# Performance work log

Measured on AMD Instinct MI355X. Metric: run time of the kernel, lower is better.

The kernel has to match this reference:

```python
import jax, jax.numpy as jnp
import numpy as np

B, N, H, E, A, V, L = 64, 196, 512, 512, 512, 20000, 20


def setup_inputs() -> dict:
    key = jax.random.key(0)
    ks = jax.random.split(key, 16)
    s = lambda *sh: 0.02
    return {
        "encoder_outputs": jax.random.normal(ks[0], (B, N, H), dtype=jnp.float32),
        "captions": jax.random.randint(ks[1], (B, L), 0, V, dtype=jnp.int64),
        "emb": jax.random.normal(ks[2], (V, E), dtype=jnp.float32) * 0.02,
        "W_ih": jax.random.normal(ks[3], (4 * H, E + H), dtype=jnp.float32) * 0.02,
        "W_hh": jax.random.normal(ks[4], (4 * H, H), dtype=jnp.float32) * 0.02,
        "b_ih": jax.random.normal(ks[5], (4 * H,), dtype=jnp.float32) * 0.02,
        "b_hh": jax.random.normal(ks[6], (4 * H,), dtype=jnp.float32) * 0.02,
        "enc_W": jax.random.normal(ks[7], (A, H), dtype=jnp.float32) * 0.02,
        "enc_b": jax.random.normal(ks[8], (A,), dtype=jnp.float32) * 0.02,
        "dec_W": jax.random.normal(ks[9], (A, H), dtype=jnp.float32) * 0.02,
        "dec_b": jax.random.normal(ks[10], (A,), dtype=jnp.float32) * 0.02,
        "energy_W": jax.random.normal(ks[11], (1, A), dtype=jnp.float32) * 0.02,
        "energy_b": jax.random.normal(ks[12], (1,), dtype=jnp.float32) * 0.02,
        "fc_W": jax.random.normal(ks[13], (V, H), dtype=jnp.float32) * 0.02,
        "fc_b": jax.random.normal(ks[14], (V,), dtype=jnp.float32) * 0.02,
    }


def reference(encoder_outputs, captions, emb, W_ih, W_hh, b_ih, b_hh,
              enc_W, enc_b, dec_W, dec_b, energy_W, energy_b, fc_W, fc_b):
    b, max_len = captions.shape
    hid = W_hh.shape[1]
    vocab = fc_W.shape[0]
    dt = encoder_outputs.dtype

    # encoder projection is hidden-state independent: hoist out of the loop
    enc_proj = jnp.einsum('bnh,ah->bna', encoder_outputs, enc_W) + enc_b  # [B,N,A]
    # teacher forcing ratio = 1.0 => input at step t is captions[:, t-1]
    emb_seq = emb[captions[:, :-1]]                                      # [B,L-1,E]
    emb_seq = jnp.swapaxes(emb_seq, 0, 1)                                # [L-1,B,E]

    def step(carry, x_t):
        h, c = carry
        dec = h @ dec_W.T + dec_b                                        # [B,A]
        scores = jnp.tanh(enc_proj + dec[:, None, :]) @ energy_W[0] + energy_b[0]  # [B,N]
        attw = jax.nn.softmax(scores, axis=1)
        context = jnp.einsum('bn,bnh->bh', attw, encoder_outputs)        # [B,H]
        lstm_in = jnp.concatenate([x_t, context], axis=1)                # [B,E+H]
        gates = lstm_in @ W_ih.T + b_ih + h @ W_hh.T + b_hh              # [B,4H]
        i, f, g, o = jnp.split(gates, 4, axis=1)
        c_new = jax.nn.sigmoid(f) * c + jax.nn.sigmoid(i) * jnp.tanh(g)
        h_new = jax.nn.sigmoid(o) * jnp.tanh(c_new)
        out = h_new @ fc_W.T + fc_b                                      # [B,V]
        return (h_new, c_new), out

    h0 = jnp.zeros((b, hid), dtype=dt)
    c0 = jnp.zeros((b, hid), dtype=dt)
    (_, _), outs = jax.lax.scan(step, (h0, c0), emb_seq)                 # [L-1,B,V]
    outputs = jnp.concatenate(
        [jnp.zeros((b, 1, vocab), dtype=dt), jnp.swapaxes(outs, 0, 1)], axis=1)
    return outputs
```

## Files before the change

### kernel.cpp

```cpp
#include <hip/hip_runtime.h>
#include <hip/hip_bf16.h>
#include <math.h>

#define B   64
#define NN  196
#define HH  512
#define EE  512
#define AA  512
#define VV  20000
#define LL  20

typedef __attribute__((ext_vector_type(8))) short bf16x8;
typedef __attribute__((ext_vector_type(4))) float floatx4;

__device__ __forceinline__ float tanh_fast(float x) {
  float e2 = __expf(2.f * x);
  return 1.f - 2.f / (e2 + 1.f);
}
__device__ __forceinline__ float sigmoid_fast(float x) {
  return 1.f / (1.f + __expf(-x));
}
__device__ __forceinline__ float bf2f(unsigned short u) {
  return __uint_as_float(((unsigned)u) << 16);
}
__device__ __forceinline__ unsigned short f2bf(float v) {
  __hip_bfloat16 h = __float2bfloat16(v);
  return *reinterpret_cast<unsigned short*>(&h);
}

__device__ __forceinline__ unsigned ald(const unsigned* p) {
  return __hip_atomic_load(p, __ATOMIC_RELAXED, __HIP_MEMORY_SCOPE_AGENT);
}
__device__ __forceinline__ void ast(unsigned* p, unsigned v) {
  __hip_atomic_store(p, v, __ATOMIC_RELAXED, __HIP_MEMORY_SCOPE_AGENT);
}
__device__ __forceinline__ int aldi(const int* p) {
  return __hip_atomic_load(p, __ATOMIC_RELAXED, __HIP_MEMORY_SCOPE_AGENT);
}
__device__ __forceinline__ void asti(int* p, int v) {
  __hip_atomic_store(p, v, __ATOMIC_RELAXED, __HIP_MEMORY_SCOPE_AGENT);
}

__device__ __forceinline__ int ldsw(int row, int q4) {
  return (row * 4 + (q4 ^ ((row >> 1) & 3))) * 8;
}
__device__ __forceinline__ int ldsw8(int row, int q8) {
  return (row * 8 + (q8 ^ (row & 7))) * 8;
}

__global__ __launch_bounds__(256) void gemm_mfma_bt(
    const unsigned short* __restrict__ Xb, const unsigned short* __restrict__ Wb,
    const float* __restrict__ bias, float* __restrict__ C,
    int M, int N, int K, int lda, int ldC, int outMode, int gridMX) {
  __shared__ unsigned short As[128 * 32];
  __shared__ unsigned short Bs[128 * 32];
  const int tid = threadIdx.x;
  const int lane = tid & 63;
  const int l15 = lane & 15;
  const int q = lane >> 4;
  const int wv = tid >> 6;
  const int wm = (wv >> 1) * 64;
  const int wn = (wv & 1) * 64;
  int mBase, nBase;
  if (gridMX == 2) {
    const int MT = (M + 127) >> 7, NT = (N + 127) >> 7;
    int wg = blockIdx.x;
    int xcd = wg & 7, idx = wg >> 3;
    int kk = idx / MT, mi = idx - kk * MT;
    int p = kk * 8 + xcd;
    if (p >= NT) return;
    mBase = mi * 128;
    nBase = p * 128;
  } else {
    mBase = blockIdx.y * 128;
    nBase = blockIdx.x * 128;
  }

  const int c0 = tid, c1 = tid + 256;
  const int r0 = c0 >> 2, q0 = c0 & 3;
  const int r1 = c1 >> 2, q1 = c1 & 3;
  const int s0 = ldsw(r0, q0), s1 = ldsw(r1, q1);

  floatx4 zero = {0.f, 0.f, 0.f, 0.f};
  floatx4 acc[4][4];
#pragma unroll
  for (int i = 0; i < 4; ++i)
#pragma unroll
    for (int j = 0; j < 4; ++j) acc[i][j] = zero;

  for (int k0 = 0; k0 < K; k0 += 32) {
    uint4 a0 = *(const uint4*)(Xb + (size_t)(mBase + r0) * lda + k0 + q0 * 8);
    uint4 a1 = *(const uint4*)(Xb + (size_t)(mBase + r1) * lda + k0 + q1 * 8);
    uint4 b0 = *(const uint4*)(Wb + (size_t)(nBase + r0) * K + k0 + q0 * 8);
    uint4 b1 = *(const uint4*)(Wb + (size_t)(nBase + r1) * K + k0 + q1 * 8);
    __syncthreads();
    *(uint4*)&As[s0] = a0;
    *(uint4*)&As[s1] = a1;
    *(uint4*)&Bs[s0] = b0;
    *(uint4*)&Bs[s1] = b1;
    __syncthreads();
    bf16x8 af[4], bfv[4];
#pragma unroll
    for (int i = 0; i < 4; ++i)
      af[i] = *(const bf16x8*)&As[ldsw(wm + i * 16 + l15, q)];
#pragma unroll
    for (int j = 0; j < 4; ++j)
      bfv[j] = *(const bf16x8*)&Bs[ldsw(wn + j * 16 + l15, q)];
#pragma unroll
    for (int i = 0; i < 4; ++i)
#pragma unroll
      for (int j = 0; j < 4; ++j)
        acc[i][j] = __builtin_amdgcn_mfma_f32_16x16x32_bf16(af[i], bfv[j],
                                                            acc[i][j], 0, 0, 0);
  }

#pragma unroll
  for (int i = 0; i < 4; ++i) {
#pragma unroll
    for (int j = 0; j < 4; ++j) {
#pragma unroll
      for (int p = 0; p < 4; ++p) {
        int m = mBase + wm + i * 16 + q * 4 + p;
        int n = nBase + wn + j * 16 + l15;
        if (m < M && n < N) {
          float v = acc[i][j][p];
          if (bias) v += bias[n];
          if (outMode == 1) {
            size_t idx = (size_t)(m & 63) * ((size_t)LL * VV) +
                         (size_t)((m >> 6) + 1) * VV + n;
            C[idx] = v;
          } else if (outMode == 2) {
            ((unsigned short*)C)[(size_t)m * ldC + n] = f2bf(v);
          } else {
            C[(size_t)m * ldC + n] = v;
          }
        }
      }
    }
  }
}

__global__ __launch_bounds__(512) void decoder_persist(
    const unsigned short* __restrict__ enc_projb,
    const unsigned short* __restrict__ encOutb,
    const unsigned short* __restrict__ dec_Wp,
    const float* __restrict__ dec_b, const float* __restrict__ eW,
    const float* __restrict__ eb,
    const unsigned short* __restrict__ Wgi,
    const float* __restrict__ gates_all_,
    float* __restrict__ c,
    unsigned short* __restrict__ xcat2,
    unsigned short* __restrict__ hb,
    int* __restrict__ flags) {
  const int tid = threadIdx.x;
  __shared__ __align__(16) char smem[58368];
  int* fctx = flags;
  int* fh = flags + 64;

  if (blockIdx.x < 64) {
    const int b = blockIdx.x;
    float* hs = (float*)smem;
    float* sdec = (float*)(smem + 2048);
    float* sw = (float*)(smem + 4096);
    float* tmp = (float*)(smem + 5120);
    float* cp = (float*)(smem + 6144);
    const int wvv = tid >> 6, lane = tid & 63;
    float ew8[8];
#pragma unroll
    for (int j = 0; j < 8; ++j) ew8[j] = eW[lane * 8 + j];
    float eb0 = eb[0];
    float dbv = dec_b[tid];

    for (int s = 0; s < 19; ++s) {
      unsigned* xc32 = (unsigned*)(xcat2 + (size_t)(s & 1) * 131072);
      if (s > 0) {
        if (tid < 16) {
          while (aldi(&fh[tid]) < s) __builtin_amdgcn_s_sleep(1);
        }
        __syncthreads();
        if (tid < 256) {
          unsigned u = ald(xc32 + (b << 9) + tid);
          hs[2 * tid] = bf2f((unsigned short)(u & 0xffffu));
          hs[2 * tid + 1] = bf2f((unsigned short)(u >> 16));
        }
      } else {
        hs[tid] = 0.f;
      }
      __syncthreads();
      {
        float dacc = dbv;
#pragma unroll 4
        for (int kg = 0; kg < 64; ++kg) {
          bf16x8 w8 = *(const bf16x8*)(dec_Wp + (size_t)((kg << 9) + tid) * 8);
#pragma unroll
          for (int j = 0; j < 8; ++j)
            dacc += hs[kg * 8 + j] * bf2f((unsigned short)w8[j]);
        }
        sdec[tid] = dacc;
      }
      __syncthreads();

      float sd8[8];
#pragma unroll
      for (int j = 0; j < 8; ++j) sd8[j] = sdec[lane * 8 + j];
      for (int n = wvv; n < NN; n += 8) {
        const unsigned short* ep =
            enc_projb + ((size_t)b * NN + n) * 512 + lane * 8;
        bf16x8 v8 = *(const bf16x8*)ep;
        float a = 0.f;
#pragma unroll
        for (int j = 0; j < 8; ++j)
          a += tanh_fast(bf2f((unsigned short)v8[j]) + sd8[j]) * ew8[j];
#pragma unroll
        for (int off = 32; off; off >>= 1) a += __shfl_down(a, off, 64);
        if (lane == 0) sw[n] = a + eb0;
      }
      __syncthreads();

      float v = (tid < NN) ? sw[tid] : -1e30f;
      if (tid < 256) tmp[tid] = v;
      __syncthreads();
      for (int st = 128; st; st >>= 1) {
        if (tid < st) tmp[tid] = fmaxf(tmp[tid], tmp[tid + st]);
        __syncthreads();
      }
      float mx = tmp[0];
      __syncthreads();
      float e = (tid < NN) ? __expf(v - mx) : 0.f;
      if (tid < 256) tmp[tid] = e;
      __syncthreads();
      for (int st = 128; st; st >>= 1) {
        if (tid < st) tmp[tid] += tmp[tid + st];
        __syncthreads();
      }
      float inv = 1.f / tmp[0];
      if (tid < NN) sw[tid] = e * inv;
      __syncthreads();

      int half = tid >> 8, hp = tid & 255;
      const unsigned short* eo = encOutb + (size_t)b * NN * 512 + hp * 2;
      float a0 = 0.f, a1 = 0.f;
      int n0 = half * 98;
#pragma unroll 7
      for (int n = n0; n < n0 + 98; ++n) {
        float w = sw[n];
        unsigned u = *(const unsigned*)(eo + (size_t)n * 512);
        a0 += w * __uint_as_float((u & 0xffffu) << 16);
        a1 += w * __uint_as_float((u >> 16) << 16);
      }
      cp[half * 512 + hp * 2] = a0;
      cp[half * 512 + hp * 2 + 1] = a1;
      __syncthreads();
      if (tid < 256) {
        float v0 = cp[2 * tid] + cp[512 + 2 * tid];
        float v1 = cp[2 * tid + 1] + cp[512 + 2 * tid + 1];
        unsigned pk = (unsigned)f2bf(v0) | ((unsigned)f2bf(v1) << 16);
        ast(xc32 + (b << 9) + 256 + tid, pk);
      }
      asm volatile("s_waitcnt vmcnt(0)" ::: "memory");
      __syncthreads();
      if (tid == 0) asti(&fctx[b], s + 1);
    }
  } else {
    const int g = blockIdx.x - 64;
    const int nBase = g * 128;
    unsigned short* As = (unsigned short*)smem;
    unsigned short* Bs = (unsigned short*)(smem + 8192);
    float(*gbuf)[132] = (float(*)[132])(smem + 24576);

    const int ar = tid >> 3, aq = tid & 7;
    const int sa = ldsw8(ar, aq);
    const int br0 = tid >> 3, bq0 = tid & 7;
    const int br1 = (tid + 512) >> 3, bq1 = tid & 7;
    const int sb0 = ldsw8(br0, bq0), sb1 = ldsw8(br1, bq1);

    const int lane = tid & 63;
    const int l15 = lane & 15;
    const int q = lane >> 4;
    const int wv = tid >> 6;
    const int wn = (wv & 3) * 32;

    for (int s = 0; s < 19; ++s) {
      unsigned* xc32 = (unsigned*)(xcat2 + (size_t)(s & 1) * 131072);
      unsigned* xn32 = (unsigned*)(xcat2 + (size_t)((s + 1) & 1) * 131072);
      const float* gx = gates_all_ + (size_t)s * 131072;
      unsigned* hb32 = (unsigned*)(hb + (size_t)s * 32768);

      if (s > 0) {
        if (tid < 16) {
          while (aldi(&fh[tid]) < s) __builtin_amdgcn_s_sleep(1);
        }
        __syncthreads();
      }

      floatx4 zero = {0.f, 0.f, 0.f, 0.f};
      floatx4 acc[4][2];
#pragma unroll
      for (int i = 0; i < 4; ++i)
#pragma unroll
        for (int j = 0; j < 2; ++j) acc[i][j] = zero;

#pragma unroll 1
      for (int ph = 0; ph < 2; ++ph) {
        if (ph == 1) {
          __syncthreads();
          if (tid < 64) {
            while (aldi(&fctx[tid]) < s + 1) __builtin_amdgcn_s_sleep(1);
          }
          __syncthreads();
        }
        const int kLo = ph * 512;
#pragma unroll 1
        for (int k0 = kLo; k0 < kLo + 512; k0 += 64) {
          const unsigned* ap = xc32 + (ar << 9) + (k0 >> 1) + aq * 4;
          unsigned au0 = ald(ap + 0);
          unsigned au1 = ald(ap + 1);
          unsigned au2 = ald(ap + 2);
          unsigned au3 = ald(ap + 3);
          uint4 b0 = *(const uint4*)(Wgi + (size_t)(nBase + br0) * 1024 + k0 +
                                     bq0 * 8);
          uint4 b1 = *(const uint4*)(Wgi + (size_t)(nBase + br1) * 1024 + k0 +
                                     bq1 * 8);
          __syncthreads();
          {
            uint4 av;
            av.x = au0; av.y = au1; av.z = au2; av.w = au3;
            *(uint4*)&As[sa] = av;
          }
          *(uint4*)&Bs[sb0] = b0;
          *(uint4*)&Bs[sb1] = b1;
          __syncthreads();
          if (tid < 256) {
#pragma unroll
            for (int ks = 0; ks < 2; ++ks) {
              bf16x8 af[4], bfv[2];
#pragma unroll
              for (int i = 0; i < 4; ++i)
                af[i] = *(const bf16x8*)&As[ldsw8(i * 16 + l15, ks * 4 + q)];
#pragma unroll
              for (int j = 0; j < 2; ++j)
                bfv[j] =
                    *(const bf16x8*)&Bs[ldsw8(wn + j * 16 + l15, ks * 4 + q)];
#pragma unroll
              for (int i = 0; i < 4; ++i)
#pragma unroll
                for (int j = 0; j < 2; ++j)
                  acc[i][j] = __builtin_amdgcn_mfma_f32_16x16x32_bf16(
                      af[i], bfv[j], acc[i][j], 0, 0, 0);
            }
          }
        }
      }

      if (tid < 256) {
#pragma unroll
        for (int i = 0; i < 4; ++i)
#pragma unroll
          for (int j = 0; j < 2; ++j)
#pragma unroll
            for (int p = 0; p < 4; ++p)
              gbuf[i * 16 + q * 4 + p][wn + j * 16 + l15] = acc[i][j][p];
      }
      __syncthreads();

#pragma unroll
      for (int it = 0; it < 2; ++it) {
        int p = it * 512 + tid;
        int bb = p >> 4, jp = p & 15;
        float4 gv0 = *(float4*)&gbuf[bb][jp * 8];
        float4 gv1 = *(float4*)&gbuf[bb][jp * 8 + 4];
        const float* gxp = gx + (size_t)bb * 2048 + nBase + jp * 8;
        float4 gx0 = *(const float4*)(gxp);
        float4 gx1 = *(const float4*)(gxp + 4);
        int jg0 = (nBase >> 2) + jp * 2;
        float cv0 = c[bb * 512 + jg0];
        float cv1 = c[bb * 512 + jg0 + 1];
        float cn0 = sigmoid_fast(gv0.y + gx0.y) * cv0 +
                    sigmoid_fast(gv0.x + gx0.x) * tanh_fast(gv0.z + gx0.z);
        float hn0 = sigmoid_fast(gv0.w + gx0.w) * tanh_fast(cn0);
        float cn1 = sigmoid_fast(gv1.y + gx1.y) * cv1 +
                    sigmoid_fast(gv1.x + gx1.x) * tanh_fast(gv1.z + gx1.z);
        float hn1 = sigmoid_fast(gv1.w + gx1.w) * tanh_fast(cn1);
        c[bb * 512 + jg0] = cn0;
        c[bb * 512 + jg0 + 1] = cn1;
        unsigned pk = (unsigned)f2bf(hn0) | ((unsigned)f2bf(hn1) << 16);
        ast(xn32 + ((bb << 10) + jg0) / 2, pk);
        hb32[((bb << 9) + jg0) / 2] = pk;
      }
      asm volatile("s_waitcnt vmcnt(0)" ::: "memory");
      __syncthreads();
      if (tid == 0) asti(&fh[g], s + 1);
    }
  }
}

#define VB_ENCOUT 2512
#define VB_WGI    4080
#define VB_WB0I   4592
#define VB_ENCW   4848
#define VB_DECW   4912
#define VB_EMB    4976
#define VB_ZOUT   5136
#define VB_CZ     5449
#define VB_XCZ    5457
#define VB_HBPAD  5489
#define VB_BSUM   5493
#define VB_TOTAL  5494

struct PrepArgs {
  const float *fc_W, *enc_out, *W_ih, *W_hh, *b_ih, *b_hh, *enc_W, *dec_W, *emb;
  const int* captions;
  unsigned short *fcWb, *encOutb, *Wgi, *Wb0i, *encWb, *dec_Wp, *embxb, *hb,
      *xcat2;
  float *bsumi, *c, *out;
  int* flags;
};

__global__ __launch_bounds__(256) void prep_all(PrepArgs A) {
  const int tid = threadIdx.x;
  const uint4 z4 = {0u, 0u, 0u, 0u};
  for (int vb = blockIdx.x; vb < VB_TOTAL; vb += gridDim.x) {
    if (vb < VB_ENCOUT) {
      int base = vb * 4096;
#pragma unroll 4
      for (int i = 0; i < 16; ++i) {
        int idx = base + i * 256 + tid;
        int r = idx >> 9, cc = idx & 511;
        float v = (r < 20000) ? A.fc_W[(size_t)r * 512 + cc] : 0.f;
        A.fcWb[idx] = f2bf(v);
      }
    } else if (vb < VB_WGI) {
      int base = (vb - VB_ENCOUT) * 4096;
#pragma unroll 4
      for (int i = 0; i < 16; ++i) {
        int idx = base + i * 256 + tid;
        A.encOutb[idx] = f2bf(A.enc_out[idx]);
      }
    } else if (vb < VB_WB0I) {
      int base = (vb - VB_WGI) * 4096;
#pragma unroll 4
      for (int i = 0; i < 16; ++i) {
        int idx = base + i * 256 + tid;
        int np = idx >> 10, k = idx & 1023;
        int row = (np & 3) * 512 + (np >> 2);
        float v = (k < 512) ? A.W_hh[(size_t)row * 512 + k]
                            : A.W_ih[(size_t)row * 1024 + 512 + (k - 512)];
        A.Wgi[idx] = f2bf(v);
      }
    } else if (vb < VB_ENCW) {
      int base = (vb - VB_WB0I) * 4096;
#pragma unroll 4
      for (int i = 0; i < 16; ++i) {
        int idx = base + i * 256 + tid;
        int np = idx >> 9, k = idx & 511;
        int row = (np & 3) * 512 + (np >> 2);
        A.Wb0i[idx] = f2bf(A.W_ih[(size_t)row * 1024 + k]);
      }
    } else if (vb < VB_DECW) {
      int base = (vb - VB_ENCW) * 4096;
#pragma unroll 4
      for (int i = 0; i < 16; ++i) {
        int idx = base + i * 256 + tid;
        A.encWb[idx] = f2bf(A.enc_W[idx]);
      }
    } else if (vb < VB_EMB) {
      int base = (vb - VB_DECW) * 4096;
#pragma unroll 4
      for (int i = 0; i < 16; ++i) {
        int idx = base + i * 256 + tid;
        int kg = idx >> 12, rem = idx & 4095;
        int a = rem >> 3, j = rem & 7;
        A.dec_Wp[idx] = f2bf(A.dec_W[(size_t)a * 512 + kg * 8 + j]);
      }
    } else if (vb < VB_ZOUT) {
      int base = (vb - VB_EMB) * 4096;
#pragma unroll 4
      for (int i = 0; i < 16; ++i) {
        int idx = base + i * 256 + tid;
        int m = idx >> 9, cc = idx & 511;
        unsigned short r = 0;
        if (m < 1216) {
          int t = m >> 6, b = m & 63;
          int cap = A.captions[b * LL + t];
          r = f2bf(A.emb[(size_t)cap * 512 + cc]);
        }
        A.embxb[idx] = r;
      }
    } else if (vb < VB_CZ) {
      int u0 = (vb - VB_ZOUT) * 1024;
      floatx4 zf = {0.f, 0.f, 0.f, 0.f};
#pragma unroll
      for (int i = 0; i < 4; ++i) {
        int u = u0 + i * 256 + tid;
        if (u < 320000) {
          int b = u / 5000, v4 = u - b * 5000;
          *(floatx4*)(A.out + (size_t)b * ((size_t)LL * VV) + v4 * 4) = zf;
        }
      }
    } else if (vb < VB_XCZ) {
      int u0 = (vb - VB_CZ) * 1024;
      floatx4 zf = {0.f, 0.f, 0.f, 0.f};
#pragma unroll
      for (int i = 0; i < 4; ++i) {
        int u = u0 + i * 256 + tid;
        *(floatx4*)(A.c + (size_t)u * 4) = zf;
      }
    } else if (vb < VB_HBPAD) {
      int u0 = (vb - VB_XCZ) * 1024;
#pragma unroll
      for (int i = 0; i < 4; ++i) {
        int u = u0 + i * 256 + tid;
        ((uint4*)A.xcat2)[u] = z4;
      }
    } else if (vb < VB_BSUM) {
      int u0 = (vb - VB_HBPAD) * 1024;
      uint4* hp = (uint4*)(A.hb + (size_t)1216 * 512);
#pragma unroll
      for (int i = 0; i < 4; ++i) {
        int u = u0 + i * 256 + tid;
        hp[u] = z4;
      }
    } else {
#pragma unroll
      for (int i = 0; i < 8; ++i) {
        int e = i * 256 + tid;
        int row = (e & 3) * 512 + (e >> 2);
        A.bsumi[e] = A.b_ih[row] + A.b_hh[row];
        if (e < 80) A.flags[e] = 0;
      }
    }
  }
}

extern "C" void kernel_launch(void* const* d_in, const int* in_sizes, int n_in,
                              void* d_out, int out_size, void* d_ws, size_t ws_size,
                              hipStream_t stream) {
  const float* enc_out  = (const float*)d_in[0];
  const int*   captions = (const int*)d_in[1];
  const float* emb      = (const float*)d_in[2];
  const float* W_ih     = (const float*)d_in[3];
  const float* W_hh     = (const float*)d_in[4];
  const float* b_ih     = (const float*)d_in[5];
  const float* b_hh     = (const float*)d_in[6];
  const float* enc_W    = (const float*)d_in[7];
  const float* enc_b    = (const float*)d_in[8];
  const float* dec_W    = (const float*)d_in[9];
  const float* dec_b    = (const float*)d_in[10];
  const float* energy_W = (const float*)d_in[11];
  const float* energy_b = (const float*)d_in[12];
  const float* fc_W     = (const float*)d_in[13];
  const float* fc_b     = (const float*)d_in[14];
  float* out = (float*)d_out;

  float* ws = (float*)d_ws;
  float* c          = ws;
  float* gates_all  = c + 32768;
  float* bsumi      = gates_all + (size_t)19 * 131072;
  int*   flags      = (int*)(bsumi + 2048);
  unsigned short* enc_projb = (unsigned short*)(flags + 80);
  unsigned short* fcWb    = enc_projb + (size_t)12544 * 512;
  unsigned short* encWb   = fcWb + (size_t)20096 * 512;
  unsigned short* encOutb = encWb + (size_t)512 * 512;
  unsigned short* Wb0i    = encOutb + (size_t)12544 * 512;
  unsigned short* Wgi     = Wb0i + (size_t)2048 * 512;
  unsigned short* dec_Wp  = Wgi + (size_t)2048 * 1024;
  unsigned short* embxb   = dec_Wp + (size_t)512 * 512;
  unsigned short* hb      = embxb + (size_t)1280 * 512;
  unsigned short* xcat2   = hb + (size_t)1280 * 512;

  PrepArgs pa;
  pa.fc_W = fc_W;     pa.enc_out = enc_out; pa.W_ih = W_ih;  pa.W_hh = W_hh;
  pa.b_ih = b_ih;     pa.b_hh = b_hh;       pa.enc_W = enc_W;
  pa.dec_W = dec_W;   pa.emb = emb;         pa.captions = captions;
  pa.fcWb = fcWb;     pa.encOutb = encOutb; pa.Wgi = Wgi;    pa.Wb0i = Wb0i;
  pa.encWb = encWb;   pa.dec_Wp = dec_Wp;   pa.embxb = embxb;
  pa.hb = hb;         pa.xcat2 = xcat2;     pa.bsumi = bsumi;
  pa.c = c;           pa.out = out;         pa.flags = flags;
  prep_all<<<2560, 256, 0, stream>>>(pa);

  gemm_mfma_bt<<<dim3(16, 10), 256, 0, stream>>>(
      embxb, Wb0i, bsumi, gates_all, 1216, 2048, 512, 512, 2048, 0, 0);

  gemm_mfma_bt<<<dim3(4, 98), 256, 0, stream>>>(
      encOutb, encWb, enc_b, (float*)enc_projb, 12544, 512, 512, 512, 512, 2, 0);

  decoder_persist<<<80, 512, 0, stream>>>(
      enc_projb, encOutb, dec_Wp, dec_b, energy_W, energy_b, Wgi, gates_all,
      c, xcat2, hb, flags);

  gemm_mfma_bt<<<1600, 256, 0, stream>>>(
      hb, fcWb, fc_b, out, 1216, 20000, 512, 512, 0, 1, 2);
}
```

Measured before the change: 1.339 ms.

## Cache enc_proj rows in LDS and software-prefetch attention and context loads

The attention blocks now copy the first 128 rows of each batch's bf16 encoder projection into a 128KB LDS buffer once, so each of the 19 steps reads them from LDS instead of global memory. The remaining rows and the context reduction use a prefetch loop that loads the next row before computing on the current one. The context sum is also regrouped so each thread accumulates 8 channels over an eighth of the positions, reduced through LDS. Step 0 skips the dec_W matvec because h is zero. The larger shared memory (150KB per block) applies to the GEMM blocks as well and may reduce occupancy or fail to fit.

```diff
diff --git a/kernel.cpp b/kernel.cpp
--- a/kernel.cpp
+++ b/kernel.cpp
@@ -153,23 +153,30 @@
     unsigned short* __restrict__ hb,
     int* __restrict__ flags) {
   const int tid = threadIdx.x;
-  __shared__ __align__(16) char smem[58368];
+  __shared__ __align__(16) char smem[153600];
   int* fctx = flags;
   int* fh = flags + 64;
 
   if (blockIdx.x < 64) {
     const int b = blockIdx.x;
-    float* hs = (float*)smem;
-    float* sdec = (float*)(smem + 2048);
-    float* sw = (float*)(smem + 4096);
-    float* tmp = (float*)(smem + 5120);
-    float* cp = (float*)(smem + 6144);
+    unsigned short* projL = (unsigned short*)smem;
+    float* hs = (float*)(smem + 131072);
+    float* sdec = (float*)(smem + 133120);
+    float* sw = (float*)(smem + 135168);
+    float* tmp = (float*)(smem + 136192);
+    float* cpR = (float*)(smem + 137216);
     const int wvv = tid >> 6, lane = tid & 63;
     float ew8[8];
 #pragma unroll
     for (int j = 0; j < 8; ++j) ew8[j] = eW[lane * 8 + j];
     float eb0 = eb[0];
     float dbv = dec_b[tid];
+
+    {
+      const uint4* src = (const uint4*)(enc_projb + (size_t)b * NN * 512);
+      uint4* dst = (uint4*)projL;
+      for (int i = tid; i < 128 * 64; i += 512) dst[i] = src[i];
+    }
 
     for (int s = 0; s < 19; ++s) {
       unsigned* xc32 = (unsigned*)(xcat2 + (size_t)(s & 1) * 131072);
@@ -183,11 +190,7 @@
           hs[2 * tid] = bf2f((unsigned short)(u & 0xffffu));
           hs[2 * tid + 1] = bf2f((unsigned short)(u >> 16));
         }
-      } else {
-        hs[tid] = 0.f;
-      }
-      __syncthreads();
-      {
+        __syncthreads();
         float dacc = dbv;
 #pragma unroll 4
         for (int kg = 0; kg < 64; ++kg) {
@@ -197,16 +200,16 @@
             dacc += hs[kg * 8 + j] * bf2f((unsigned short)w8[j]);
         }
         sdec[tid] = dacc;
+      } else {
+        sdec[tid] = dbv;
       }
       __syncthreads();
 
       float sd8[8];
 #pragma unroll
       for (int j = 0; j < 8; ++j) sd8[j] = sdec[lane * 8 + j];
-      for (int n = wvv; n < NN; n += 8) {
-        const unsigned short* ep =
-            enc_projb + ((size_t)b * NN + n) * 512 + lane * 8;
-        bf16x8 v8 = *(const bf16x8*)ep;
+      for (int n = wvv; n < 128; n += 8) {
+        bf16x8 v8 = *(const bf16x8*)&projL[n * 512 + lane * 8];
         float a = 0.f;
 #pragma unroll
         for (int j = 0; j < 8; ++j)
@@ -214,6 +217,28 @@
 #pragma unroll
         for (int off = 32; off; off >>= 1) a += __shfl_down(a, off, 64);
         if (lane == 0) sw[n] = a + eb0;
+      }
+      {
+        const unsigned short* epb =
+            enc_projb + (size_t)b * NN * 512 + lane * 8;
+        int n = 128 + wvv;
+        bf16x8 v8 = *(const bf16x8*)(epb + (size_t)n * 512);
+#pragma unroll 1
+        while (true) {
+          int n2 = n + 8;
+          bf16x8 vnx = v8;
+          if (n2 < NN) vnx = *(const bf16x8*)(epb + (size_t)n2 * 512);
+          float a = 0.f;
+#pragma unroll
+          for (int j = 0; j < 8; ++j)
+            a += tanh_fast(bf2f((unsigned short)v8[j]) + sd8[j]) * ew8[j];
+#pragma unroll
+          for (int off = 32; off; off >>= 1) a += __shfl_down(a, off, 64);
+          if (lane == 0) sw[n] = a + eb0;
+          v8 = vnx;
+          n = n2;
+          if (n >= NN) break;
+        }
       }
       __syncthreads();
 
@@ -237,23 +262,40 @@
       if (tid < NN) sw[tid] = e * inv;
       __syncthreads();
 
-      int half = tid >> 8, hp = tid & 255;
-      const unsigned short* eo = encOutb + (size_t)b * NN * 512 + hp * 2;
-      float a0 = 0.f, a1 = 0.f;
-      int n0 = half * 98;
-#pragma unroll 7
-      for (int n = n0; n < n0 + 98; ++n) {
-        float w = sw[n];
-        unsigned u = *(const unsigned*)(eo + (size_t)n * 512);
-        a0 += w * __uint_as_float((u & 0xffffu) << 16);
-        a1 += w * __uint_as_float((u >> 16) << 16);
-      }
-      cp[half * 512 + hp * 2] = a0;
-      cp[half * 512 + hp * 2 + 1] = a1;
+      {
+        const int st = tid >> 6;
+        const int cg = tid & 63;
+        float a[8] = {0.f, 0.f, 0.f, 0.f, 0.f, 0.f, 0.f, 0.f};
+        const unsigned short* eo =
+            encOutb + (size_t)b * NN * 512 + cg * 8;
+        int n = st;
+        bf16x8 v8 = *(const bf16x8*)(eo + (size_t)n * 512);
+#pragma unroll 1
+        while (true) {
+          int n2 = n + 8;
+          bf16x8 vnx = v8;
+          if (n2 < NN) vnx = *(const bf16x8*)(eo + (size_t)n2 * 512);
+          float w = sw[n];
+#pragma unroll
+          for (int j = 0; j < 8; ++j)
+            a[j] += w * bf2f((unsigned short)v8[j]);
+          v8 = vnx;
+          n = n2;
+          if (n >= NN) break;
+        }
+        floatx4 a0v = {a[0], a[1], a[2], a[3]};
+        floatx4 a1v = {a[4], a[5], a[6], a[7]};
+        *(floatx4*)&cpR[st * 512 + cg * 8] = a0v;
+        *(floatx4*)&cpR[st * 512 + cg * 8 + 4] = a1v;
+      }
       __syncthreads();
       if (tid < 256) {
-        float v0 = cp[2 * tid] + cp[512 + 2 * tid];
-        float v1 = cp[2 * tid + 1] + cp[512 + 2 * tid + 1];
+        float v0 = 0.f, v1 = 0.f;
+#pragma unroll
+        for (int st = 0; st < 8; ++st) {
+          v0 += cpR[st * 512 + 2 * tid];
+          v1 += cpR[st * 512 + 2 * tid + 1];
+        }
         unsigned pk = (unsigned)f2bf(v0) | ((unsigned)f2bf(v1) << 16);
         ast(xc32 + (b << 9) + 256 + tid, pk);
       }
```

Result: no change. 1.334 ms (-0.3%).
